# Kernel optimization log

Hardware: AMD Instinct MI355X
Metric: run time of the kernel (lower is better)

The kernel has to match this reference:

```python
import jax, jax.numpy as jnp
import numpy as np

EMBED_DIM = 1024
NUM_HEADS = 16
HEAD_DIM = EMBED_DIM // NUM_HEADS


def setup_inputs() -> dict:
    key = jax.random.key(0)
    k_x, k_wqkv, k_bqkv, k_wout, k_bout = jax.random.split(key, 5)
    B, T, C = 2, 2048, EMBED_DIM
    s = 1.0 / np.sqrt(C)
    return {
        "x": jax.random.normal(k_x, (B, T, C), dtype=jnp.float32),
        "W_qkv": jax.random.uniform(k_wqkv, (C, 3 * C), jnp.float32, -s, s),
        "b_qkv": jax.random.uniform(k_bqkv, (3 * C,), jnp.float32, -s, s),
        "W_out": jax.random.uniform(k_wout, (C, C), jnp.float32, -s, s),
        "b_out": jax.random.uniform(k_bout, (C,), jnp.float32, -s, s),
    }


def reference(x, W_qkv, b_qkv, W_out, b_out):
    B, T, C = x.shape
    H, D = NUM_HEADS, HEAD_DIM
    qkv = x @ W_qkv + b_qkv                      # [B,T,3C]
    # Faithful to torch: reshape to [B,T,H,3D], move heads, chunk last dim.
    qkv = qkv.reshape(B, T, H, 3 * D).transpose(0, 2, 1, 3)  # [B,H,T,3D]
    q, k, v = qkv[..., :D], qkv[..., D:2 * D], qkv[..., 2 * D:]
    scores = jnp.einsum("bhqd,bhkd->bhqk", q, k) / np.sqrt(D).astype(jnp.float32)
    weights = jax.nn.softmax(scores, axis=-1)    # [B,H,T,T]
    attn = jnp.einsum("bhqk,bhkd->bhqd", weights, v)  # [B,H,T,D]
    attn = attn.transpose(0, 2, 1, 3).reshape(B, T, C)
    return attn @ W_out + b_out
```

## Files before the change

kernel.cpp:

```cpp
#include <hip/hip_runtime.h>


typedef float  f32x4  __attribute__((ext_vector_type(4)));
typedef __bf16 bf16x8 __attribute__((ext_vector_type(8)));

#define QSCALE 0.18033688011112042f

#if __has_builtin(__builtin_amdgcn_exp2f)
#define EXP2(x) __builtin_amdgcn_exp2f(x)
#else
#define EXP2(x) exp2f(x)
#endif
#if __has_builtin(__builtin_amdgcn_rcpf)
#define RCP(x) __builtin_amdgcn_rcpf(x)
#else
#define RCP(x) (1.0f / (x))
#endif

static __device__ __forceinline__ f32x4 mfma32(bf16x8 a, bf16x8 b, f32x4 c) {
    return __builtin_amdgcn_mfma_f32_16x16x32_bf16(a, b, c, 0, 0, 0);
}

static __device__ __forceinline__ bf16x8 ld8(const unsigned short* p) {
    return __builtin_bit_cast(bf16x8, *(const uint4*)p);
}
static __device__ __forceinline__ unsigned short bfbits(float f) {
    __bf16 h = (__bf16)f;
    return __builtin_bit_cast(unsigned short, h);
}

static __device__ __forceinline__ void glds16(const unsigned short* g,
                                              unsigned short* lds_base) {
    __builtin_amdgcn_global_load_lds(
        (const __attribute__((address_space(1))) unsigned int*)g,
        (__attribute__((address_space(3))) unsigned int*)lds_base, 16, 0, 0);
}

__global__ __launch_bounds__(256) void prep_kernel(
    const float* __restrict__ x, unsigned short* __restrict__ xb,
    const float* __restrict__ Wqkv, unsigned short* __restrict__ wqkvT,
    const float* __restrict__ Wout, unsigned short* __restrict__ woutT) {
    __shared__ float tile[32][33];
    const int bid = blockIdx.x;
    if (bid < 4096) {
        int i = bid * 256 + threadIdx.x;
        float4 v = ((const float4*)x)[i];
        ushort4 o;
        o.x = bfbits(v.x); o.y = bfbits(v.y);
        o.z = bfbits(v.z); o.w = bfbits(v.w);
        ((ushort4*)xb)[i] = o;
        return;
    }
    const float* W; unsigned short* Wt; int N, n0, k0;
    if (bid < 7168) {
        int l = bid - 4096; W = Wqkv; Wt = wqkvT; N = 3072;
        n0 = (l % 96) * 32; k0 = (l / 96) * 32;
    } else {
        int l = bid - 7168; W = Wout; Wt = woutT; N = 1024;
        n0 = (l & 31) * 32; k0 = (l >> 5) * 32;
    }
    int tx = threadIdx.x & 31, ty = threadIdx.x >> 5;
#pragma unroll
    for (int i = 0; i < 4; i++) {
        int r = ty + i * 8;
        tile[r][tx] = W[(size_t)(k0 + r) * N + n0 + tx];
    }
    __syncthreads();
#pragma unroll
    for (int i = 0; i < 4; i++) {
        int r = ty + i * 8;
        Wt[(size_t)(n0 + r) * 1024 + k0 + tx] = bfbits(tile[tx][r]);
    }
}

__global__ __launch_bounds__(256) void qkv_gemm_kernel(
    const unsigned short* __restrict__ A, const unsigned short* __restrict__ Bt,
    const float* __restrict__ bias, unsigned short* __restrict__ Qb,
    unsigned short* __restrict__ Kb, unsigned short* __restrict__ Vtb) {
    __shared__ unsigned short As[3][128 * 32];
    __shared__ unsigned short Bs[3][128 * 32];
    const int wg = blockIdx.x;
    const int xcd = wg & 7, local = wg >> 3;
    const int n_t = (xcd >> 2) * 12 + local % 12;
    const int m_t = (xcd & 3) * 8 + local / 12;
    const int m0 = m_t * 128, n0 = n_t * 128;
    const int tid = threadIdx.x;
    const int lane = tid & 63, w = tid >> 6;
    const int ln = lane & 15, quad = lane >> 4;
    const int wm = (w >> 1) * 64, wn = (w & 1) * 64;
    const int sr = lane >> 2, sc = (lane & 3) * 8;

    const unsigned short* a_rd = &As[0][(wm + ln) * 32 + quad * 8];
    const unsigned short* b_rd = &Bs[0][(wn + ln) * 32 + quad * 8];
    unsigned short* a_st0 = &As[0][(w * 32) * 32];
    unsigned short* a_st1 = &As[0][(w * 32 + 16) * 32];
    unsigned short* b_st0 = &Bs[0][(w * 32) * 32];
    unsigned short* b_st1 = &Bs[0][(w * 32 + 16) * 32];
    const unsigned short* Ag0 = &A[(size_t)(m0 + w * 32 + sr) * 1024 + sc];
    const unsigned short* Ag1 = &A[(size_t)(m0 + w * 32 + 16 + sr) * 1024 + sc];
    const unsigned short* Bg0 = &Bt[(size_t)(n0 + w * 32 + sr) * 1024 + sc];
    const unsigned short* Bg1 = &Bt[(size_t)(n0 + w * 32 + 16 + sr) * 1024 + sc];

#define QSTAGE(OFF, KC)                                                       \
    do {                                                                      \
        glds16(Ag0 + (KC), a_st0 + (OFF));                                    \
        glds16(Bg0 + (KC), b_st0 + (OFF));                                    \
        glds16(Ag1 + (KC), a_st1 + (OFF));                                    \
        glds16(Bg1 + (KC), b_st1 + (OFF));                                    \
    } while (0)

#define QCOMPUTE(CO)                                                          \
    do {                                                                      \
        bf16x8 af[4], bf[4];                                                  \
        _Pragma("unroll")                                                     \
        for (int mi = 0; mi < 4; mi++)                                        \
            af[mi] = ld8(a_rd + (CO) + mi * 512);                             \
        _Pragma("unroll")                                                     \
        for (int ni = 0; ni < 4; ni++)                                        \
            bf[ni] = ld8(b_rd + (CO) + ni * 512);                             \
        __builtin_amdgcn_s_setprio(1);                                        \
        _Pragma("unroll")                                                     \
        for (int mi = 0; mi < 4; mi++)                                        \
            _Pragma("unroll")                                                 \
            for (int ni = 0; ni < 4; ni++)                                    \
                acc[mi][ni] = mfma32(af[mi], bf[ni], acc[mi][ni]);            \
        __builtin_amdgcn_s_setprio(0);                                        \
    } while (0)

    f32x4 acc[4][4] = {};
    QSTAGE(0, 0);
    QSTAGE(4096, 32);
    int co = 0;
    int so = 2 * 4096;
    for (int kt = 0; kt < 31; kt++) {
        asm volatile("s_waitcnt vmcnt(4)" ::: "memory");
        __builtin_amdgcn_sched_barrier(0);
        asm volatile("s_barrier" ::: "memory");
        __builtin_amdgcn_sched_barrier(0);
        if (kt + 2 < 32) QSTAGE(so, (kt + 2) * 32);
        QCOMPUTE(co);
        co = (co == 2 * 4096) ? 0 : co + 4096;
        so = (so == 2 * 4096) ? 0 : so + 4096;
    }
    asm volatile("s_waitcnt vmcnt(0)" ::: "memory");
    __builtin_amdgcn_sched_barrier(0);
    asm volatile("s_barrier" ::: "memory");
    __builtin_amdgcn_sched_barrier(0);
    QCOMPUTE(co);
#undef QSTAGE
#undef QCOMPUTE

#pragma unroll
    for (int mi = 0; mi < 4; mi++)
#pragma unroll
        for (int ni = 0; ni < 4; ni++) {
            int gn = n0 + wn + ni * 16 + ln;
            float bi = bias[gn];
            int h = gn / 192, rr = gn - h * 192;
            int gm0 = m0 + wm + mi * 16 + quad * 4;
            int b = gm0 >> 11, t0 = gm0 & 2047;
            float vv[4];
#pragma unroll
            for (int r = 0; r < 4; r++) vv[r] = acc[mi][ni][r] + bi;
            if (rr < 64) {
                size_t base = ((size_t)(b * 16 + h) * 2048 + t0) * 64 + rr;
#pragma unroll
                for (int r = 0; r < 4; r++)
                    Qb[base + (size_t)r * 64] = bfbits(vv[r] * QSCALE);
            } else if (rr < 128) {
                size_t base = ((size_t)(b * 16 + h) * 2048 + t0) * 64 + rr - 64;
#pragma unroll
                for (int r = 0; r < 4; r++)
                    Kb[base + (size_t)r * 64] = bfbits(vv[r]);
            } else {
                int tp0 = (t0 & ~31) | (quad << 3) | ((mi & 1) << 2);
                ushort4 pk;
                pk.x = bfbits(vv[0]); pk.y = bfbits(vv[1]);
                pk.z = bfbits(vv[2]); pk.w = bfbits(vv[3]);
                *(ushort4*)&Vtb[((size_t)(b * 16 + h) * 64 + (rr - 128)) * 2048
                                + tp0] = pk;
            }
        }
}

__global__ __launch_bounds__(512)
__attribute__((amdgpu_waves_per_eu(4, 4)))
void attn_kernel(
    const unsigned short* __restrict__ Q, const unsigned short* __restrict__ K,
    const unsigned short* __restrict__ Vt, unsigned short* __restrict__ Ob) {
    __shared__ unsigned short smem[2][2][2][4096];
    const int wg  = blockIdx.x;
    const int xcd = wg & 7, local = wg >> 3;
    const int bh  = xcd * 4 + (local >> 4);
    const int qt  = local & 15;
    const int tid = threadIdx.x;
    const int lane = tid & 63, w = tid >> 6;
    const int w4 = w & 3, ks = w >> 2;
    const int ln = lane & 15, quad = lane >> 4;
    const int lr = lane >> 3, lg = lane & 7;
    const int e = ln & 7;

    unsigned short (*Ks)[4096] = smem[ks][0];
    unsigned short (*Vs)[4096] = smem[ks][1];

    const unsigned short* Qg = Q + ((size_t)bh * 2048 + qt * 128) * 64;
    const unsigned short* Kg = K + ((size_t)bh * 2048 + ks * 1024) * 64;
    const unsigned short* Vg = Vt + (size_t)bh * 64 * 2048 + ks * 1024;

    bf16x8 qf[2][2];
#pragma unroll
    for (int h = 0; h < 2; h++) {
        const unsigned short* qp = Qg + (size_t)(w4 * 32 + h * 16 + ln) * 64;
        qf[h][0] = ld8(qp + quad * 8);
        qf[h][1] = ld8(qp + 32 + quad * 8);
    }

    const unsigned short* kb0 = &Ks[0][ln * 64 + (quad ^ e) * 8];
    const unsigned short* kb1 = &Ks[0][ln * 64 + ((4 + quad) ^ e) * 8];
    const unsigned short* vp0 = &Vs[0][ln * 64 + (quad ^ e) * 8];
    const unsigned short* vp1 = &Vs[0][ln * 64 + ((4 + quad) ^ e) * 8];

    const int kof0 = (w4 * 16 + lr) * 64 + (lg ^ lr) * 8;
    const int kof1 = (w4 * 16 + 8 + lr) * 64 + (lg ^ lr) * 8;
    const int vof0 = (w4 * 16 + lr) * 2048 + (lg ^ lr) * 8;
    const int vof1 = (w4 * 16 + 8 + lr) * 2048 + (lg ^ lr) * 8;
    unsigned short* kd0[2] = {&Ks[0][(w4 * 16) * 64], &Ks[1][(w4 * 16) * 64]};
    unsigned short* kd1[2] = {&Ks[0][(w4 * 16 + 8) * 64], &Ks[1][(w4 * 16 + 8) * 64]};
    unsigned short* vd0[2] = {&Vs[0][(w4 * 16) * 64], &Vs[1][(w4 * 16) * 64]};
    unsigned short* vd1[2] = {&Vs[0][(w4 * 16 + 8) * 64], &Vs[1][(w4 * 16 + 8) * 64]};

    glds16(Kg + kof0, kd0[0]);
    glds16(Kg + kof1, kd1[0]);
    glds16(Vg + vof0, vd0[0]);
    glds16(Vg + vof1, vd1[0]);
    __syncthreads();

    const unsigned short* KgR = Kg + 4096;
    const unsigned short* VgR = Vg + 64;

    bf16x8 ones8;
#pragma unroll
    for (int j = 0; j < 8; j++) ones8[j] = __bf16(1.0f);
    f32x4 zero4 = {};
    asm volatile("" : "+v"(zero4));
    f32x4 o[2][4] = {};
    f32x4 lacc[2] = {};

#define ATTN_TILE(CUR, PREF)                                                  \
    do {                                                                      \
        if (PREF) {                                                           \
            glds16(KgR + kof0, kd0[CUR ^ 1]);                                 \
            glds16(KgR + kof1, kd1[CUR ^ 1]);                                 \
            glds16(VgR + vof0, vd0[CUR ^ 1]);                                 \
            glds16(VgR + vof1, vd1[CUR ^ 1]);                                 \
            KgR += 4096; VgR += 64;                                           \
        }                                                                     \
        f32x4 s[2][4];                                                        \
        __builtin_amdgcn_s_setprio(1);                                        \
        _Pragma("unroll")                                                     \
        for (int ms = 0; ms < 4; ms++) {                                      \
            bf16x8 a0 = ld8(kb0 + (CUR) * 4096 + ms * 1024);                  \
            bf16x8 a1 = ld8(kb1 + (CUR) * 4096 + ms * 1024);                  \
            _Pragma("unroll")                                                 \
            for (int h = 0; h < 2; h++) {                                     \
                s[h][ms] = mfma32(a0, qf[h][0], zero4);                       \
                s[h][ms] = mfma32(a1, qf[h][1], s[h][ms]);                    \
            }                                                                 \
        }                                                                     \
        __builtin_amdgcn_s_setprio(0);                                        \
        bf16x8 pb8[2][2];                                                     \
        _Pragma("unroll")                                                     \
        for (int h = 0; h < 2; h++)                                           \
            _Pragma("unroll")                                                 \
            for (int p = 0; p < 2; p++) {                                     \
                f32x4 e0, e1;                                                 \
                e0[0] = EXP2(s[h][2 * p][0]); e0[1] = EXP2(s[h][2 * p][1]);   \
                e0[2] = EXP2(s[h][2 * p][2]); e0[3] = EXP2(s[h][2 * p][3]);   \
                e1[0] = EXP2(s[h][2 * p + 1][0]);                             \
                e1[1] = EXP2(s[h][2 * p + 1][1]);                             \
                e1[2] = EXP2(s[h][2 * p + 1][2]);                             \
                e1[3] = EXP2(s[h][2 * p + 1][3]);                             \
                pb8[h][p][0] = __bf16(e0[0]); pb8[h][p][1] = __bf16(e0[1]);   \
                pb8[h][p][2] = __bf16(e0[2]); pb8[h][p][3] = __bf16(e0[3]);   \
                pb8[h][p][4] = __bf16(e1[0]); pb8[h][p][5] = __bf16(e1[1]);   \
                pb8[h][p][6] = __bf16(e1[2]); pb8[h][p][7] = __bf16(e1[3]);   \
            }                                                                 \
        __builtin_amdgcn_s_setprio(1);                                        \
        _Pragma("unroll")                                                     \
        for (int h = 0; h < 2; h++)                                           \
            _Pragma("unroll")                                                 \
            for (int p = 0; p < 2; p++)                                       \
                lacc[h] = mfma32(ones8, pb8[h][p], lacc[h]);                  \
        _Pragma("unroll")                                                     \
        for (int df = 0; df < 4; df++) {                                      \
            bf16x8 a80 = ld8(vp0 + (CUR) * 4096 + df * 1024);                 \
            o[0][df] = mfma32(a80, pb8[0][0], o[0][df]);                      \
            o[1][df] = mfma32(a80, pb8[1][0], o[1][df]);                      \
            bf16x8 a81 = ld8(vp1 + (CUR) * 4096 + df * 1024);                 \
            o[0][df] = mfma32(a81, pb8[0][1], o[0][df]);                      \
            o[1][df] = mfma32(a81, pb8[1][1], o[1][df]);                      \
        }                                                                     \
        __builtin_amdgcn_s_setprio(0);                                        \
        __syncthreads();                                                      \
    } while (0)

    for (int it = 0; it < 8; it++) {
        ATTN_TILE(0, true);
        ATTN_TILE(1, (it < 7));
    }
#undef ATTN_TILE

    float* xf = (float*)&smem[0][0][0][0];
    const int slot = w4 * 64 + lane;
    if (ks) {
#pragma unroll
        for (int h = 0; h < 2; h++)
#pragma unroll
            for (int df = 0; df < 4; df++) {
                int j = h * 4 + df;
                *(f32x4*)(xf + (size_t)(slot * 8 + (j ^ (slot & 7))) * 4) = o[h][df];
            }
        xf[8192 + slot * 2 + 0] = lacc[0][0];
        xf[8192 + slot * 2 + 1] = lacc[1][0];
    }
    __syncthreads();
    if (!ks) {
        float inv0 = RCP(lacc[0][0] + xf[8192 + slot * 2 + 0]);
        float inv1 = RCP(lacc[1][0] + xf[8192 + slot * 2 + 1]);
        const int b = bh >> 4, hh = bh & 15;
#pragma unroll
        for (int h = 0; h < 2; h++) {
            float inv = h ? inv1 : inv0;
            int qrow = qt * 128 + w4 * 32 + h * 16 + ln;
            size_t row = ((size_t)b * 2048 + qrow) * 1024 + hh * 64;
#pragma unroll
            for (int df = 0; df < 4; df++) {
                int j = h * 4 + df;
                f32x4 oo = *(const f32x4*)(xf + (size_t)(slot * 8 + (j ^ (slot & 7))) * 4);
                ushort4 pk;
                pk.x = bfbits((o[h][df][0] + oo[0]) * inv);
                pk.y = bfbits((o[h][df][1] + oo[1]) * inv);
                pk.z = bfbits((o[h][df][2] + oo[2]) * inv);
                pk.w = bfbits((o[h][df][3] + oo[3]) * inv);
                *(ushort4*)&Ob[row + df * 16 + quad * 4] = pk;
            }
        }
    }
}

__global__ __launch_bounds__(256) void out_gemm_kernel(
    const unsigned short* __restrict__ A, const unsigned short* __restrict__ Bt,
    const float* __restrict__ bias, float* __restrict__ out) {
    __shared__ unsigned short As[2][64 * 32];
    __shared__ unsigned short Bs[2][128 * 32];
    const int wg = blockIdx.x;
    const int xcd = wg & 7, local = wg >> 3;
    const int m_t = xcd * 8 + (local & 7);
    const int n_t = local >> 3;
    const int m0 = m_t * 64, n0 = n_t * 128;
    const int tid = threadIdx.x;
    const int lane = tid & 63, w = tid >> 6;
    const int ln = lane & 15, quad = lane >> 4;
    const int wm = (w >> 1) * 32, wn = (w & 1) * 64;
    const int sr = lane >> 2, sc = (lane & 3) * 8;
    f32x4 acc[2][4] = {};
    {
        int ra = w * 16;
        glds16(&A[(size_t)(m0 + ra + sr) * 1024 + sc], &As[0][ra * 32]);
#pragma unroll
        for (int i = 0; i < 2; i++) {
            int rb = w * 32 + i * 16;
            glds16(&Bt[(size_t)(n0 + rb + sr) * 1024 + sc], &Bs[0][rb * 32]);
        }
    }
    __syncthreads();
    for (int kt = 0; kt < 32; kt++) {
        const int cur = kt & 1;
        if (kt + 1 < 32) {
            const int nxt = cur ^ 1;
            const int kc = (kt + 1) * 32;
            int ra = w * 16;
            glds16(&A[(size_t)(m0 + ra + sr) * 1024 + kc + sc], &As[nxt][ra * 32]);
#pragma unroll
            for (int i = 0; i < 2; i++) {
                int rb = w * 32 + i * 16;
                glds16(&Bt[(size_t)(n0 + rb + sr) * 1024 + kc + sc], &Bs[nxt][rb * 32]);
            }
        }
        bf16x8 af[2], bf[4];
#pragma unroll
        for (int mi = 0; mi < 2; mi++)
            af[mi] = ld8(&As[cur][(wm + mi * 16 + ln) * 32 + quad * 8]);
#pragma unroll
        for (int ni = 0; ni < 4; ni++)
            bf[ni] = ld8(&Bs[cur][(wn + ni * 16 + ln) * 32 + quad * 8]);
#pragma unroll
        for (int mi = 0; mi < 2; mi++)
#pragma unroll
            for (int ni = 0; ni < 4; ni++)
                acc[mi][ni] = mfma32(af[mi], bf[ni], acc[mi][ni]);
        __syncthreads();
    }
#pragma unroll
    for (int mi = 0; mi < 2; mi++)
#pragma unroll
        for (int ni = 0; ni < 4; ni++) {
            int gn = n0 + wn + ni * 16 + ln;
            float bi = bias[gn];
#pragma unroll
            for (int r = 0; r < 4; r++) {
                int gm = m0 + wm + mi * 16 + quad * 4 + r;
                out[(size_t)gm * 1024 + gn] = acc[mi][ni][r] + bi;
            }
        }
}

extern "C" void kernel_launch(void* const* d_in, const int* in_sizes, int n_in,
                              void* d_out, int out_size, void* d_ws, size_t ws_size,
                              hipStream_t stream) {
    const float* x     = (const float*)d_in[0];
    const float* W_qkv = (const float*)d_in[1];
    const float* b_qkv = (const float*)d_in[2];
    const float* W_out = (const float*)d_in[3];
    const float* b_out = (const float*)d_in[4];
    float* out = (float*)d_out;

    char* ws = (char*)d_ws;
    unsigned short* xb    = (unsigned short*)(ws);
    unsigned short* wqkvT = (unsigned short*)(ws + (size_t)( 8 << 20));
    unsigned short* woutT = (unsigned short*)(ws + (size_t)(14 << 20));
    unsigned short* Qb    = (unsigned short*)(ws + (size_t)(16 << 20));
    unsigned short* Kb    = (unsigned short*)(ws + (size_t)(24 << 20));
    unsigned short* Vtb   = (unsigned short*)(ws + (size_t)(32 << 20));
    unsigned short* attnb = (unsigned short*)(ws + (size_t)(40 << 20));

    prep_kernel<<<8192, 256, 0, stream>>>(x, xb, W_qkv, wqkvT, W_out, woutT);
    qkv_gemm_kernel<<<768, 256, 0, stream>>>(xb, wqkvT, b_qkv, Qb, Kb, Vtb);
    attn_kernel<<<512, 512, 0, stream>>>(Qb, Kb, Vtb, attnb);
    out_gemm_kernel<<<512, 256, 0, stream>>>(attnb, woutT, b_out, out);
}
```

Measured before the change: 171.6 us.

## Use partial vmcnt waits with raw barriers and triple-buffer the output GEMM

In the attention loop, the full __syncthreads is replaced with explicit s_waitcnt vmcnt(4)/vmcnt(0) plus raw s_barrier, so the prefetch of the next K/V tile can stay in flight while the current tile is computed. The output projection GEMM moves from a double to a triple-buffered LDS pipeline with two stages in flight. It uses partial vmcnt waits, precomputed base pointers and setprio around the MFMAs. The aim is to hide global-to-LDS load latency, at the cost of more LDS and correctness that depends on exact vmcnt counting.

After: 174.6 us. Within noise of the previous version (+1.8%).

```diff
diff --git a/kernel.cpp b/kernel.cpp
--- a/kernel.cpp
+++ b/kernel.cpp
@@ -255,6 +255,11 @@
             glds16(VgR + vof1, vd1[CUR ^ 1]);                                 \
             KgR += 4096; VgR += 64;                                           \
         }                                                                     \
+        if (PREF) { asm volatile("s_waitcnt vmcnt(4)" ::: "memory"); }        \
+        else      { asm volatile("s_waitcnt vmcnt(0)" ::: "memory"); }        \
+        __builtin_amdgcn_sched_barrier(0);                                    \
+        asm volatile("s_barrier" ::: "memory");                               \
+        __builtin_amdgcn_sched_barrier(0);                                    \
         f32x4 s[2][4];                                                        \
         __builtin_amdgcn_s_setprio(1);                                        \
         _Pragma("unroll")                                                     \
@@ -301,13 +306,17 @@
             o[1][df] = mfma32(a81, pb8[1][1], o[1][df]);                      \
         }                                                                     \
         __builtin_amdgcn_s_setprio(0);                                        \
-        __syncthreads();                                                      \
+        __builtin_amdgcn_sched_barrier(0);                                    \
+        asm volatile("s_barrier" ::: "memory");                               \
+        __builtin_amdgcn_sched_barrier(0);                                    \
     } while (0)
 
-    for (int it = 0; it < 8; it++) {
-        ATTN_TILE(0, true);
-        ATTN_TILE(1, (it < 7));
-    }
+    for (int it = 0; it < 7; it++) {
+        ATTN_TILE(0, 1);
+        ATTN_TILE(1, 1);
+    }
+    ATTN_TILE(0, 1);
+    ATTN_TILE(1, 0);
 #undef ATTN_TILE
 
     float* xf = (float*)&smem[0][0][0][0];
@@ -351,8 +360,8 @@
 __global__ __launch_bounds__(256) void out_gemm_kernel(
     const unsigned short* __restrict__ A, const unsigned short* __restrict__ Bt,
     const float* __restrict__ bias, float* __restrict__ out) {
-    __shared__ unsigned short As[2][64 * 32];
-    __shared__ unsigned short Bs[2][128 * 32];
+    __shared__ unsigned short As[3][64 * 32];
+    __shared__ unsigned short Bs[3][128 * 32];
     const int wg = blockIdx.x;
     const int xcd = wg & 7, local = wg >> 3;
     const int m_t = xcd * 8 + (local & 7);
@@ -363,44 +372,66 @@
     const int ln = lane & 15, quad = lane >> 4;
     const int wm = (w >> 1) * 32, wn = (w & 1) * 64;
     const int sr = lane >> 2, sc = (lane & 3) * 8;
+
+    const unsigned short* Ag = &A[(size_t)(m0 + w * 16 + sr) * 1024 + sc];
+    const unsigned short* Bg0 = &Bt[(size_t)(n0 + w * 32 + sr) * 1024 + sc];
+    const unsigned short* Bg1 = &Bt[(size_t)(n0 + w * 32 + 16 + sr) * 1024 + sc];
+    unsigned short* a_st = &As[0][(w * 16) * 32];
+    unsigned short* b_st0 = &Bs[0][(w * 32) * 32];
+    unsigned short* b_st1 = &Bs[0][(w * 32 + 16) * 32];
+    const unsigned short* a_rd = &As[0][(wm + ln) * 32 + quad * 8];
+    const unsigned short* b_rd = &Bs[0][(wn + ln) * 32 + quad * 8];
+
+#define OSTAGE(AO, BO, KC)                                                    \
+    do {                                                                      \
+        glds16(Ag + (KC), a_st + (AO));                                       \
+        glds16(Bg0 + (KC), b_st0 + (BO));                                     \
+        glds16(Bg1 + (KC), b_st1 + (BO));                                     \
+    } while (0)
+
+#define OCOMPUTE(AO, BO)                                                      \
+    do {                                                                      \
+        bf16x8 af[2], bf[4];                                                  \
+        _Pragma("unroll")                                                     \
+        for (int mi = 0; mi < 2; mi++)                                        \
+            af[mi] = ld8(a_rd + (AO) + mi * 512);                             \
+        _Pragma("unroll")                                                     \
+        for (int ni = 0; ni < 4; ni++)                                        \
+            bf[ni] = ld8(b_rd + (BO) + ni * 512);                             \
+        __builtin_amdgcn_s_setprio(1);                                        \
+        _Pragma("unroll")                                                     \
+        for (int mi = 0; mi < 2; mi++)                                        \
+            _Pragma("unroll")                                                 \
+            for (int ni = 0; ni < 4; ni++)                                    \
+                acc[mi][ni] = mfma32(af[mi], bf[ni], acc[mi][ni]);            \
+        __builtin_amdgcn_s_setprio(0);                                        \
+    } while (0)
+
     f32x4 acc[2][4] = {};
-    {
-        int ra = w * 16;
-        glds16(&A[(size_t)(m0 + ra + sr) * 1024 + sc], &As[0][ra * 32]);
-#pragma unroll
-        for (int i = 0; i < 2; i++) {
-            int rb = w * 32 + i * 16;
-            glds16(&Bt[(size_t)(n0 + rb + sr) * 1024 + sc], &Bs[0][rb * 32]);
-        }
-    }
-    __syncthreads();
-    for (int kt = 0; kt < 32; kt++) {
-        const int cur = kt & 1;
-        if (kt + 1 < 32) {
-            const int nxt = cur ^ 1;
-            const int kc = (kt + 1) * 32;
-            int ra = w * 16;
-            glds16(&A[(size_t)(m0 + ra + sr) * 1024 + kc + sc], &As[nxt][ra * 32]);
-#pragma unroll
-            for (int i = 0; i < 2; i++) {
-                int rb = w * 32 + i * 16;
-                glds16(&Bt[(size_t)(n0 + rb + sr) * 1024 + kc + sc], &Bs[nxt][rb * 32]);
-            }
-        }
-        bf16x8 af[2], bf[4];
-#pragma unroll
-        for (int mi = 0; mi < 2; mi++)
-            af[mi] = ld8(&As[cur][(wm + mi * 16 + ln) * 32 + quad * 8]);
-#pragma unroll
-        for (int ni = 0; ni < 4; ni++)
-            bf[ni] = ld8(&Bs[cur][(wn + ni * 16 + ln) * 32 + quad * 8]);
-#pragma unroll
-        for (int mi = 0; mi < 2; mi++)
-#pragma unroll
-            for (int ni = 0; ni < 4; ni++)
-                acc[mi][ni] = mfma32(af[mi], bf[ni], acc[mi][ni]);
-        __syncthreads();
-    }
+    OSTAGE(0, 0, 0);
+    OSTAGE(2048, 4096, 32);
+    int ao = 0, bo = 0;
+    int as = 2 * 2048, bs = 2 * 4096;
+    for (int kt = 0; kt < 31; kt++) {
+        asm volatile("s_waitcnt vmcnt(3)" ::: "memory");
+        __builtin_amdgcn_sched_barrier(0);
+        asm volatile("s_barrier" ::: "memory");
+        __builtin_amdgcn_sched_barrier(0);
+        if (kt + 2 < 32) OSTAGE(as, bs, (kt + 2) * 32);
+        OCOMPUTE(ao, bo);
+        ao = (ao == 2 * 2048) ? 0 : ao + 2048;
+        bo = (bo == 2 * 4096) ? 0 : bo + 4096;
+        as = (as == 2 * 2048) ? 0 : as + 2048;
+        bs = (bs == 2 * 4096) ? 0 : bs + 4096;
+    }
+    asm volatile("s_waitcnt vmcnt(0)" ::: "memory");
+    __builtin_amdgcn_sched_barrier(0);
+    asm volatile("s_barrier" ::: "memory");
+    __builtin_amdgcn_sched_barrier(0);
+    OCOMPUTE(ao, bo);
+#undef OSTAGE
+#undef OCOMPUTE
+
 #pragma unroll
     for (int mi = 0; mi < 2; mi++)
 #pragma unroll
```
